# Kernel optimization log

Hardware: AMD Instinct MI355X
Metric: run time of the kernel (lower is better)

## Reference

```python
import jax, jax.numpy as jnp
import numpy as np

B, S, D, H, V, C = 64, 512, 512, 512, 32000, 1000
FF = 1024

def setup_inputs() -> dict:
    key = jax.random.key(0)
    ks = jax.random.split(key, 12)
    s = 0.02
    return {
        "tokens": jax.random.randint(ks[0], (B, S), 0, V),
        "emb": jax.random.normal(ks[1], (V, D), jnp.float32) * s,
        "Wx": jax.random.normal(ks[2], (D, H), jnp.float32) * s,
        "Wh": jax.random.normal(ks[3], (H, H), jnp.float32) * s,
        "b_rnn": jnp.zeros((H,), jnp.float32),
        "W1": jax.random.normal(ks[4], (H, FF), jnp.float32) * s,
        "b1": jnp.zeros((FF,), jnp.float32),
        "W2": jax.random.normal(ks[5], (FF, FF), jnp.float32) * s,
        "b2": jnp.zeros((FF,), jnp.float32),
        "Wo": jax.random.normal(ks[6], (FF, C), jnp.float32) * s,
        "bo": jnp.zeros((C,), jnp.float32),
    }

def reference(tokens, emb, Wx, Wh, b_rnn, W1, b1, W2, b2, Wo, bo):
    # Embedding with mask_zero=True: token 0 is a masked timestep
    x = emb[tokens]                                   # [B,S,D]
    mask = (tokens != 0)                              # [B,S]
    # Precompute input projection for all timesteps (hoisted out of the scan)
    xproj = jnp.einsum('bsd,dh->bsh', x, Wx) + b_rnn  # [B,S,H]

    def step(h, inp):
        xp, m = inp                                   # [B,H], [B]
        h_new = jax.nn.relu(xp + h @ Wh)
        # Keras masking: masked steps carry previous state forward
        h = jnp.where(m[:, None], h_new, h)
        return h, None

    h0 = jnp.zeros((B, H), xproj.dtype)
    h, _ = jax.lax.scan(step, h0, (xproj.transpose(1, 0, 2), mask.T))

    y = jax.nn.relu(h @ W1 + b1)
    y = jax.nn.relu(y @ W2 + b2)
    return jax.nn.softmax(y @ Wo + bo, axis=-1)       # [B,C]
```

## Files before the change

### kernel.cpp

```cpp
#include <hip/hip_runtime.h>
#include <stdint.h>

typedef _Float16 half2_t __attribute__((ext_vector_type(2)));
typedef short bf16x8 __attribute__((ext_vector_type(8)));
typedef float f32x4 __attribute__((ext_vector_type(4)));
typedef int i32x4 __attribute__((ext_vector_type(4)));
typedef int i32x8 __attribute__((ext_vector_type(8)));
typedef unsigned short u16;
typedef unsigned int u32;
typedef unsigned long long u64;

#define B_ 64
#define S_ 512
#define D_ 512
#define H_ 512
#define FF_ 1024
#define C_ 1000
#define V_ 32000

#define SW4 128.0f
#define SH4 256.0f

__device__ __forceinline__ u16 f2bf(float f){
  u32 u = __builtin_bit_cast(u32, f);
  u = (u + 0x7FFFu + ((u >> 16) & 1u)) >> 16;
  return (u16)u;
}
__device__ __forceinline__ u32 pkbf(float a, float b){
  return (u32)f2bf(a) | ((u32)f2bf(b) << 16);
}
__device__ __forceinline__ u32 packh2(float a, float b){
  u16 lo = __builtin_bit_cast(u16, (_Float16)a);
  u16 hi = __builtin_bit_cast(u16, (_Float16)b);
  return (u32)lo | ((u32)hi << 16);
}
__device__ __forceinline__ float fdot2u(u32 a, u32 b, float c){
  return __builtin_amdgcn_fdot2(__builtin_bit_cast(half2_t, a),
                                __builtin_bit_cast(half2_t, b), c, false);
}
__device__ __forceinline__ float h2f(u16 h){
  return (float)__builtin_bit_cast(_Float16, h);
}
__device__ __forceinline__ float fp4val(u32 c){
  int e = (c >> 1) & 3;
  float m = 1.0f + 0.5f * (float)(c & 1);
  return (e == 0) ? 0.5f * (float)(c & 1) : m * (float)(1 << (e - 1));
}

__global__ void k_prep(const float* __restrict__ Wx, u16* __restrict__ WxT,
                       const float* __restrict__ Wh, uint4* __restrict__ Wf4){
  __shared__ u16 t[64][65];
  int bid = blockIdx.x, tid = threadIdx.x;
  if (bid < 64){
    int bx = bid & 7, by = bid >> 3;
    int c = tid & 63, r0 = (tid >> 6) * 16;
    #pragma unroll
    for (int i = 0; i < 16; i++){
      int k = by * 64 + r0 + i, n = bx * 64 + c;
      t[r0 + i][c] = f2bf(Wx[k * 512 + n]);
    }
    __syncthreads();
    #pragma unroll
    for (int i = 0; i < 16; i++){
      int n = bx * 64 + r0 + i, k = by * 64 + c;
      WxT[n * 512 + k] = t[c][r0 + i];
    }
  } else {
    int g = (bid - 64) * 256 + tid;
    int fidx = g >> 6, l = g & 63;
    int wv = fidx >> 4, ct = (fidx >> 2) & 3, kt = fidx & 3;
    int q = l >> 4, n = wv * 64 + ct * 16 + (l & 15);
    int k0 = kt * 128 + q * 32;
    u32 d[4] = {0u, 0u, 0u, 0u};
    #pragma unroll
    for (int j = 0; j < 32; j++){
      float w = Wh[(size_t)(k0 + j) * 512 + n] * SW4;
      float aw = fabsf(w);
      u32 s = (w < 0.f) ? 8u : 0u;
      u32 c;
      if (aw < 2.f) c = (u32)(int)rintf(aw * 2.f);
      else if (aw < 4.f) c = 4u + (u32)(int)rintf(aw - 2.f);
      else { c = 6u + (u32)(int)rintf((aw - 4.f) * 0.5f); if (c > 7u) c = 7u; }
      d[j >> 3] |= (c | s) << (4 * (j & 7));
    }
    uint4 o; o.x = d[0]; o.y = d[1]; o.z = d[2]; o.w = d[3];
    Wf4[(size_t)fidx * 64 + l] = o;
  }
}

__global__ __launch_bounds__(512) void k_gemm(const float* __restrict__ emb,
                                              const u16* __restrict__ WxT,
                                              const float* __restrict__ bias,
                                              u16* __restrict__ xpV,
                                              const float* __restrict__ W1, u32* __restrict__ W1p,
                                              const float* __restrict__ W2, u32* __restrict__ W2p,
                                              const float* __restrict__ Wo, u32* __restrict__ Wop){
  __shared__ __align__(16) u16 As[64 * 40];
  int bid = blockIdx.x, tid = threadIdx.x;
  if (bid >= 500){
    if (bid < 1012){
      int i = (bid - 500) * 512 + tid;
      int p = i >> 10, n = i & 1023;
      W1p[p * FF_ + n] = packh2(W1[(2 * p) * FF_ + n], W1[(2 * p + 1) * FF_ + n]);
    } else if (bid < 2036){
      int i = (bid - 1012) * 512 + tid;
      int p = i >> 10, n = i & 1023;
      W2p[p * FF_ + n] = packh2(W2[(2 * p) * FF_ + n], W2[(2 * p + 1) * FF_ + n]);
    } else {
      int i = (bid - 2036) * 512 + tid;
      int p = i >> 10, n = i & 1023;
      if (n < C_)
        Wop[p * C_ + n] = packh2(Wo[(2 * p) * C_ + n], Wo[(2 * p + 1) * C_ + n]);
    }
    return;
  }
  int m0 = bid * 64;
  int w = tid >> 6, l = tid & 63, kg = l >> 4, r16 = l & 15;
  const u16* bptr[4];
  #pragma unroll
  for (int ni = 0; ni < 4; ni++)
    bptr[ni] = WxT + (size_t)(w * 64 + ni * 16 + r16) * 512 + kg * 8;
  f32x4 acc[4][4];
  #pragma unroll
  for (int mi = 0; mi < 4; mi++)
    #pragma unroll
    for (int ni = 0; ni < 4; ni++) acc[mi][ni] = (f32x4){0.f, 0.f, 0.f, 0.f};
  int srow = tid >> 3, sk = (tid & 7) * 4;
  const float* ebase = emb + (size_t)(m0 + srow) * 512 + sk;
  float4 f = *(const float4*)ebase;
  for (int kt = 0; kt < 16; kt++){
    u32 lo = pkbf(f.x, f.y), hi = pkbf(f.z, f.w);
    float4 fn;
    if (kt < 15) fn = *(const float4*)(ebase + (kt + 1) * 32);
    __syncthreads();
    uint2 st; st.x = lo; st.y = hi;
    *(uint2*)(As + srow * 40 + sk) = st;
    __syncthreads();
    bf16x8 bfr[4], af[4];
    #pragma unroll
    for (int ni = 0; ni < 4; ni++)
      bfr[ni] = *(const bf16x8*)(bptr[ni] + kt * 32);
    #pragma unroll
    for (int mi = 0; mi < 4; mi++)
      af[mi] = *(const bf16x8*)(As + (mi * 16 + r16) * 40 + kg * 8);
    #pragma unroll
    for (int mi = 0; mi < 4; mi++)
      #pragma unroll
      for (int ni = 0; ni < 4; ni++)
        acc[mi][ni] = __builtin_amdgcn_mfma_f32_16x16x32_bf16(af[mi], bfr[ni], acc[mi][ni], 0, 0, 0);
    f = fn;
  }
  #pragma unroll
  for (int ni = 0; ni < 4; ni++){
    int col = w * 64 + ni * 16 + r16;
    float bb = bias[col];
    #pragma unroll
    for (int mi = 0; mi < 4; mi++){
      int mb = m0 + mi * 16 + kg * 4;
      #pragma unroll
      for (int r = 0; r < 4; r++){
        float v = (acc[mi][ni][r] + bb) * SH4;
        xpV[(size_t)(mb + r) * 512 + col] = __builtin_bit_cast(u16, (_Float16)v);
      }
    }
  }
}

__global__ __launch_bounds__(512, 2) void k_rnn(
    const uint4* __restrict__ Wf4, const u16* __restrict__ xpV,
    const int* __restrict__ tokens, u32* __restrict__ hpack){
  __shared__ __align__(16) unsigned char gA[256];
  __shared__ __align__(16) unsigned char gB[256];
  __shared__ int toks[512];
  int b = blockIdx.x, tid = threadIdx.x;
  int wv = tid >> 6, l = tid & 63, q = l >> 4, n16 = l & 15;
  int col = wv * 64 + q * 16 + n16;

  i32x8 wgt[16];
  #pragma unroll
  for (int ct = 0; ct < 4; ct++)
    #pragma unroll
    for (int kt = 0; kt < 4; kt++){
      int fidx = (wv * 4 + ct) * 4 + kt;
      uint4 wl = Wf4[(size_t)fidx * 64 + l];
      i32x8 w8 = {(int)wl.x, (int)wl.y, (int)wl.z, (int)wl.w, 0, 0, 0, 0};
      wgt[ct * 4 + kt] = w8;
    }

  toks[tid] = tokens[b * 512 + tid];
  if (tid < 64) ((u32*)gA)[tid] = 0;
  __syncthreads();

  const u16* xpc = xpV + col;
  u16 xraw = xpc[(size_t)toks[0] * 512];
  u32 greg = 0;

#define RNN_STEP(T, SRC, DST)                                                 \
  {                                                                           \
    int tn = toks[(T + 1) & 511];                                             \
    u16 xnext = xpc[(size_t)tn * 512];                                        \
    bool wr = toks[T] != 0;                                                   \
    i32x4 av0 = *(const i32x4*)(SRC + 0 * 64 + q * 16);                       \
    i32x4 av1 = *(const i32x4*)(SRC + 1 * 64 + q * 16);                       \
    i32x4 av2 = *(const i32x4*)(SRC + 2 * 64 + q * 16);                       \
    i32x4 av3 = *(const i32x4*)(SRC + 3 * 64 + q * 16);                       \
    i32x8 a80 = {av0[0], av0[1], av0[2], av0[3], 0, 0, 0, 0};                 \
    i32x8 a81 = {av1[0], av1[1], av1[2], av1[3], 0, 0, 0, 0};                 \
    i32x8 a82 = {av2[0], av2[1], av2[2], av2[3], 0, 0, 0, 0};                 \
    i32x8 a83 = {av3[0], av3[1], av3[2], av3[3], 0, 0, 0, 0};                 \
    f32x4 acc0 = {0.f,0.f,0.f,0.f}, acc1 = {0.f,0.f,0.f,0.f};                 \
    f32x4 acc2 = {0.f,0.f,0.f,0.f}, acc3 = {0.f,0.f,0.f,0.f};                 \
    __builtin_amdgcn_s_setprio(1);                                            \
    acc0 = __builtin_amdgcn_mfma_scale_f32_16x16x128_f8f6f4(a80, wgt[0],  acc0, 4, 4, 0, 127, 0, 127); \
    acc1 = __builtin_amdgcn_mfma_scale_f32_16x16x128_f8f6f4(a80, wgt[4],  acc1, 4, 4, 0, 127, 0, 127); \
    acc2 = __builtin_amdgcn_mfma_scale_f32_16x16x128_f8f6f4(a80, wgt[8],  acc2, 4, 4, 0, 127, 0, 127); \
    acc3 = __builtin_amdgcn_mfma_scale_f32_16x16x128_f8f6f4(a80, wgt[12], acc3, 4, 4, 0, 127, 0, 127); \
    acc0 = __builtin_amdgcn_mfma_scale_f32_16x16x128_f8f6f4(a81, wgt[1],  acc0, 4, 4, 0, 127, 0, 127); \
    acc1 = __builtin_amdgcn_mfma_scale_f32_16x16x128_f8f6f4(a81, wgt[5],  acc1, 4, 4, 0, 127, 0, 127); \
    acc2 = __builtin_amdgcn_mfma_scale_f32_16x16x128_f8f6f4(a81, wgt[9],  acc2, 4, 4, 0, 127, 0, 127); \
    acc3 = __builtin_amdgcn_mfma_scale_f32_16x16x128_f8f6f4(a81, wgt[13], acc3, 4, 4, 0, 127, 0, 127); \
    acc0 = __builtin_amdgcn_mfma_scale_f32_16x16x128_f8f6f4(a82, wgt[2],  acc0, 4, 4, 0, 127, 0, 127); \
    acc1 = __builtin_amdgcn_mfma_scale_f32_16x16x128_f8f6f4(a82, wgt[6],  acc1, 4, 4, 0, 127, 0, 127); \
    acc2 = __builtin_amdgcn_mfma_scale_f32_16x16x128_f8f6f4(a82, wgt[10], acc2, 4, 4, 0, 127, 0, 127); \
    acc3 = __builtin_amdgcn_mfma_scale_f32_16x16x128_f8f6f4(a82, wgt[14], acc3, 4, 4, 0, 127, 0, 127); \
    acc0 = __builtin_amdgcn_mfma_scale_f32_16x16x128_f8f6f4(a83, wgt[3],  acc0, 4, 4, 0, 127, 0, 127); \
    acc1 = __builtin_amdgcn_mfma_scale_f32_16x16x128_f8f6f4(a83, wgt[7],  acc1, 4, 4, 0, 127, 0, 127); \
    acc2 = __builtin_amdgcn_mfma_scale_f32_16x16x128_f8f6f4(a83, wgt[11], acc2, 4, 4, 0, 127, 0, 127); \
    acc3 = __builtin_amdgcn_mfma_scale_f32_16x16x128_f8f6f4(a83, wgt[15], acc3, 4, 4, 0, 127, 0, 127); \
    __builtin_amdgcn_s_setprio(0);                                            \
    float av = (q == 0) ? acc0[0] : (q == 1) ? acc1[0] : (q == 2) ? acc2[0] : acc3[0]; \
    float gn = fmaxf(fmaf(av, 1.0f / SW4, h2f(xraw)), 0.f);                   \
    u32 code;                                                                 \
    if (gn < 2.f) code = (u32)(int)rintf(gn * 2.f);                           \
    else if (gn < 4.f) code = 4u + (u32)(int)rintf(gn - 2.f);                 \
    else { u32 c = 6u + (u32)(int)rintf((gn - 4.f) * 0.5f); code = c > 7u ? 7u : c; } \
    u32 pc = (u32)__shfl_xor((int)code, 1);                                   \
    u32 byte = (n16 & 1) ? (pc | (code << 4)) : (code | (pc << 4));           \
    if (wr) greg = byte;                                                      \
    if ((l & 1) == 0) DST[col >> 1] = (unsigned char)greg;                    \
    xraw = xnext;                                                             \
  }

  #pragma unroll 1
  for (int t = 0; t < 512; t += 2){
    RNN_STEP(t, gA, gB);
    __syncthreads();
    RNN_STEP(t + 1, gB, gA);
    __syncthreads();
  }
#undef RNN_STEP

  if (tid < 256){
    u32 byte = gA[tid];
    float f0 = fp4val(byte & 15u) * (1.0f / SH4);
    float f1 = fp4val(byte >> 4) * (1.0f / SH4);
    hpack[b * 256 + tid] = packh2(f0, f1);
  }
}

__global__ __launch_bounds__(256) void k_fc1(const u32* __restrict__ hpack,
    const u32* __restrict__ W1p, const float* __restrict__ b1, u32* __restrict__ y1p){
  __shared__ u32 h0[256], h1[256];
  int nx = blockIdx.x, bp = blockIdx.y, tid = threadIdx.x;
  int ba = bp * 2, bb = ba + 1;
  int n = nx * 256 + tid;
  h0[tid] = hpack[ba * 256 + tid];
  h1[tid] = hpack[bb * 256 + tid];
  __syncthreads();
  float a0 = 0.f, a1 = 0.f;
  #pragma unroll 8
  for (int p = 0; p < 256; p++){
    u32 w = W1p[p * FF_ + n];
    a0 = fdot2u(w, h0[p], a0);
    a1 = fdot2u(w, h1[p], a1);
  }
  float bbv = b1[n];
  float y0 = fmaxf(a0 + bbv, 0.f), y1 = fmaxf(a1 + bbv, 0.f);
  float o0 = __shfl_xor(y0, 1), o1 = __shfl_xor(y1, 1);
  if (!(tid & 1)){
    y1p[ba * 512 + (n >> 1)] = packh2(y0, o0);
    y1p[bb * 512 + (n >> 1)] = packh2(y1, o1);
  }
}

__global__ __launch_bounds__(256) void k_fc2(const u32* __restrict__ y1p,
    const u32* __restrict__ W2p, const float* __restrict__ b2, u32* __restrict__ y2p){
  __shared__ u32 h0[512], h1[512];
  int nx = blockIdx.x, bp = blockIdx.y, tid = threadIdx.x;
  int ba = bp * 2, bb = ba + 1;
  int n = nx * 256 + tid;
  h0[tid] = y1p[ba * 512 + tid];       h1[tid] = y1p[bb * 512 + tid];
  h0[tid + 256] = y1p[ba * 512 + 256 + tid];
  h1[tid + 256] = y1p[bb * 512 + 256 + tid];
  __syncthreads();
  float a0 = 0.f, a1 = 0.f;
  #pragma unroll 8
  for (int p = 0; p < 512; p++){
    u32 w = W2p[p * FF_ + n];
    a0 = fdot2u(w, h0[p], a0);
    a1 = fdot2u(w, h1[p], a1);
  }
  float bbv = b2[n];
  float y0 = fmaxf(a0 + bbv, 0.f), y1 = fmaxf(a1 + bbv, 0.f);
  float o0 = __shfl_xor(y0, 1), o1 = __shfl_xor(y1, 1);
  if (!(tid & 1)){
    y2p[ba * 512 + (n >> 1)] = packh2(y0, o0);
    y2p[bb * 512 + (n >> 1)] = packh2(y1, o1);
  }
}

__global__ __launch_bounds__(256) void k_outz(const u32* __restrict__ y2p,
    const u32* __restrict__ Wop, const float* __restrict__ bo, float* __restrict__ z){
  __shared__ u32 h0[512], h1[512];
  int nx = blockIdx.x, bp = blockIdx.y, tid = threadIdx.x;
  int ba = bp * 2, bb = ba + 1;
  h0[tid] = y2p[ba * 512 + tid];       h1[tid] = y2p[bb * 512 + tid];
  h0[tid + 256] = y2p[ba * 512 + 256 + tid];
  h1[tid + 256] = y2p[bb * 512 + 256 + tid];
  __syncthreads();
  int n = nx * 250 + tid;
  if (tid >= 250) return;
  float a0 = 0.f, a1 = 0.f;
  #pragma unroll 8
  for (int p = 0; p < 512; p++){
    u32 w = Wop[p * C_ + n];
    a0 = fdot2u(w, h0[p], a0);
    a1 = fdot2u(w, h1[p], a1);
  }
  float bbv = bo[n];
  z[ba * C_ + n] = a0 + bbv;
  z[bb * C_ + n] = a1 + bbv;
}

__global__ __launch_bounds__(256) void k_norm(const float* __restrict__ z,
                                              float* __restrict__ out){
  __shared__ float redm[4], reds[4];
  int b = blockIdx.x, tid = threadIdx.x;
  float z0 = z[b * C_ + tid];
  float z1 = z[b * C_ + 256 + tid];
  float z2 = z[b * C_ + 512 + tid];
  bool v3 = (768 + tid) < C_;
  float z3 = v3 ? z[b * C_ + 768 + tid] : -1e30f;
  float mx = fmaxf(fmaxf(z0, z1), fmaxf(z2, z3));
  #pragma unroll
  for (int o = 1; o < 64; o <<= 1) mx = fmaxf(mx, __shfl_xor(mx, o));
  if ((tid & 63) == 0) redm[tid >> 6] = mx;
  __syncthreads();
  mx = fmaxf(fmaxf(redm[0], redm[1]), fmaxf(redm[2], redm[3]));
  float e0 = __expf(z0 - mx), e1 = __expf(z1 - mx), e2 = __expf(z2 - mx);
  float e3 = v3 ? __expf(z3 - mx) : 0.f;
  float s = e0 + e1 + e2 + e3;
  #pragma unroll
  for (int o = 1; o < 64; o <<= 1) s += __shfl_xor(s, o);
  if ((tid & 63) == 0) reds[tid >> 6] = s;
  __syncthreads();
  s = reds[0] + reds[1] + reds[2] + reds[3];
  float inv = 1.0f / s;
  out[b * C_ + tid] = e0 * inv;
  out[b * C_ + 256 + tid] = e1 * inv;
  out[b * C_ + 512 + tid] = e2 * inv;
  if (v3) out[b * C_ + 768 + tid] = e3 * inv;
}

extern "C" void kernel_launch(void* const* d_in, const int* in_sizes, int n_in,
                              void* d_out, int out_size, void* d_ws, size_t ws_size,
                              hipStream_t stream) {
  const int*   tokens = (const int*)d_in[0];
  const float* emb    = (const float*)d_in[1];
  const float* Wx     = (const float*)d_in[2];
  const float* Wh     = (const float*)d_in[3];
  const float* brnn   = (const float*)d_in[4];
  const float* W1     = (const float*)d_in[5];
  const float* b1     = (const float*)d_in[6];
  const float* W2     = (const float*)d_in[7];
  const float* b2     = (const float*)d_in[8];
  const float* Wo     = (const float*)d_in[9];
  const float* bo     = (const float*)d_in[10];
  float* out = (float*)d_out;

  char* ws = (char*)d_ws;
  size_t off = 0;
  auto alloc = [&](size_t bytes) -> void* {
    void* p = ws + off;
    off += (bytes + 255) & ~(size_t)255;
    return p;
  };
  u16* WxT    = (u16*)alloc((size_t)512 * 512 * 2);
  u16* xpV    = (u16*)alloc((size_t)V_ * 512 * 2);
  uint4* Wf4  = (uint4*)alloc((size_t)128 * 64 * 16);
  u32* W1p    = (u32*)alloc((size_t)256 * 1024 * 4);
  u32* W2p    = (u32*)alloc((size_t)512 * 1024 * 4);
  u32* Wop    = (u32*)alloc((size_t)512 * 1000 * 4);
  u32* hpack  = (u32*)alloc((size_t)64 * 256 * 4);
  u32* y1p    = (u32*)alloc((size_t)64 * 512 * 4);
  u32* y2p    = (u32*)alloc((size_t)64 * 512 * 4);
  float* zbuf = (float*)alloc((size_t)64 * 1000 * 4);

  k_prep<<<dim3(96), dim3(256), 0, stream>>>(Wx, WxT, Wh, Wf4);
  k_gemm<<<dim3(3060), dim3(512), 0, stream>>>(emb, WxT, brnn, xpV,
                                               W1, W1p, W2, W2p, Wo, Wop);
  k_rnn<<<dim3(64), dim3(512), 0, stream>>>(Wf4, xpV, tokens, hpack);
  k_fc1<<<dim3(4, 32), dim3(256), 0, stream>>>(hpack, W1p, b1, y1p);
  k_fc2<<<dim3(4, 32), dim3(256), 0, stream>>>(y1p, W2p, b2, y2p);
  k_outz<<<dim3(4, 32), dim3(256), 0, stream>>>(y2p, Wop, bo, zbuf);
  k_norm<<<dim3(64), dim3(256), 0, stream>>>(zbuf, out);
}
```

Before: 377.3 us.

## Switch RNN hidden state to FP8 and fuse MLP tail into one grid-barrier kernel

```diff
diff --git a/kernel.cpp b/kernel.cpp
--- a/kernel.cpp
+++ b/kernel.cpp
@@ -40,11 +40,6 @@
 }
 __device__ __forceinline__ float h2f(u16 h){
   return (float)__builtin_bit_cast(_Float16, h);
-}
-__device__ __forceinline__ float fp4val(u32 c){
-  int e = (c >> 1) & 3;
-  float m = 1.0f + 0.5f * (float)(c & 1);
-  return (e == 0) ? 0.5f * (float)(c & 1) : m * (float)(1 << (e - 1));
 }
 
 __global__ void k_prep(const float* __restrict__ Wx, u16* __restrict__ WxT,
@@ -94,10 +89,12 @@
                                               u16* __restrict__ xpV,
                                               const float* __restrict__ W1, u32* __restrict__ W1p,
                                               const float* __restrict__ W2, u32* __restrict__ W2p,
-                                              const float* __restrict__ Wo, u32* __restrict__ Wop){
+                                              const float* __restrict__ Wo, u32* __restrict__ Wop,
+                                              u32* __restrict__ sync){
   __shared__ __align__(16) u16 As[64 * 40];
   int bid = blockIdx.x, tid = threadIdx.x;
   if (bid >= 500){
+    if (bid == 500 && tid < 8) sync[tid] = 0;
     if (bid < 1012){
       int i = (bid - 500) * 512 + tid;
       int p = i >> 10, n = i & 1023;
@@ -169,8 +166,8 @@
 __global__ __launch_bounds__(512, 2) void k_rnn(
     const uint4* __restrict__ Wf4, const u16* __restrict__ xpV,
     const int* __restrict__ tokens, u32* __restrict__ hpack){
-  __shared__ __align__(16) unsigned char gA[256];
-  __shared__ __align__(16) unsigned char gB[256];
+  __shared__ __align__(32) unsigned char gA[512];
+  __shared__ __align__(32) unsigned char gB[512];
   __shared__ int toks[512];
   int b = blockIdx.x, tid = threadIdx.x;
   int wv = tid >> 6, l = tid & 63, q = l >> 4, n16 = l & 15;
@@ -188,7 +185,7 @@
     }
 
   toks[tid] = tokens[b * 512 + tid];
-  if (tid < 64) ((u32*)gA)[tid] = 0;
+  if (tid < 128) ((u32*)gA)[tid] = 0;
   __syncthreads();
 
   const u16* xpc = xpV + col;
@@ -200,44 +197,35 @@
     int tn = toks[(T + 1) & 511];                                             \
     u16 xnext = xpc[(size_t)tn * 512];                                        \
     bool wr = toks[T] != 0;                                                   \
-    i32x4 av0 = *(const i32x4*)(SRC + 0 * 64 + q * 16);                       \
-    i32x4 av1 = *(const i32x4*)(SRC + 1 * 64 + q * 16);                       \
-    i32x4 av2 = *(const i32x4*)(SRC + 2 * 64 + q * 16);                       \
-    i32x4 av3 = *(const i32x4*)(SRC + 3 * 64 + q * 16);                       \
-    i32x8 a80 = {av0[0], av0[1], av0[2], av0[3], 0, 0, 0, 0};                 \
-    i32x8 a81 = {av1[0], av1[1], av1[2], av1[3], 0, 0, 0, 0};                 \
-    i32x8 a82 = {av2[0], av2[1], av2[2], av2[3], 0, 0, 0, 0};                 \
-    i32x8 a83 = {av3[0], av3[1], av3[2], av3[3], 0, 0, 0, 0};                 \
+    i32x8 a80 = *(const i32x8*)(SRC + 0 * 128 + q * 32);                      \
+    i32x8 a81 = *(const i32x8*)(SRC + 1 * 128 + q * 32);                      \
+    i32x8 a82 = *(const i32x8*)(SRC + 2 * 128 + q * 32);                      \
+    i32x8 a83 = *(const i32x8*)(SRC + 3 * 128 + q * 32);                      \
     f32x4 acc0 = {0.f,0.f,0.f,0.f}, acc1 = {0.f,0.f,0.f,0.f};                 \
     f32x4 acc2 = {0.f,0.f,0.f,0.f}, acc3 = {0.f,0.f,0.f,0.f};                 \
     __builtin_amdgcn_s_setprio(1);                                            \
-    acc0 = __builtin_amdgcn_mfma_scale_f32_16x16x128_f8f6f4(a80, wgt[0],  acc0, 4, 4, 0, 127, 0, 127); \
-    acc1 = __builtin_amdgcn_mfma_scale_f32_16x16x128_f8f6f4(a80, wgt[4],  acc1, 4, 4, 0, 127, 0, 127); \
-    acc2 = __builtin_amdgcn_mfma_scale_f32_16x16x128_f8f6f4(a80, wgt[8],  acc2, 4, 4, 0, 127, 0, 127); \
-    acc3 = __builtin_amdgcn_mfma_scale_f32_16x16x128_f8f6f4(a80, wgt[12], acc3, 4, 4, 0, 127, 0, 127); \
-    acc0 = __builtin_amdgcn_mfma_scale_f32_16x16x128_f8f6f4(a81, wgt[1],  acc0, 4, 4, 0, 127, 0, 127); \
-    acc1 = __builtin_amdgcn_mfma_scale_f32_16x16x128_f8f6f4(a81, wgt[5],  acc1, 4, 4, 0, 127, 0, 127); \
-    acc2 = __builtin_amdgcn_mfma_scale_f32_16x16x128_f8f6f4(a81, wgt[9],  acc2, 4, 4, 0, 127, 0, 127); \
-    acc3 = __builtin_amdgcn_mfma_scale_f32_16x16x128_f8f6f4(a81, wgt[13], acc3, 4, 4, 0, 127, 0, 127); \
-    acc0 = __builtin_amdgcn_mfma_scale_f32_16x16x128_f8f6f4(a82, wgt[2],  acc0, 4, 4, 0, 127, 0, 127); \
-    acc1 = __builtin_amdgcn_mfma_scale_f32_16x16x128_f8f6f4(a82, wgt[6],  acc1, 4, 4, 0, 127, 0, 127); \
-    acc2 = __builtin_amdgcn_mfma_scale_f32_16x16x128_f8f6f4(a82, wgt[10], acc2, 4, 4, 0, 127, 0, 127); \
-    acc3 = __builtin_amdgcn_mfma_scale_f32_16x16x128_f8f6f4(a82, wgt[14], acc3, 4, 4, 0, 127, 0, 127); \
-    acc0 = __builtin_amdgcn_mfma_scale_f32_16x16x128_f8f6f4(a83, wgt[3],  acc0, 4, 4, 0, 127, 0, 127); \
-    acc1 = __builtin_amdgcn_mfma_scale_f32_16x16x128_f8f6f4(a83, wgt[7],  acc1, 4, 4, 0, 127, 0, 127); \
-    acc2 = __builtin_amdgcn_mfma_scale_f32_16x16x128_f8f6f4(a83, wgt[11], acc2, 4, 4, 0, 127, 0, 127); \
-    acc3 = __builtin_amdgcn_mfma_scale_f32_16x16x128_f8f6f4(a83, wgt[15], acc3, 4, 4, 0, 127, 0, 127); \
+    acc0 = __builtin_amdgcn_mfma_scale_f32_16x16x128_f8f6f4(a80, wgt[0],  acc0, 0, 4, 0, 127, 0, 127); \
+    acc1 = __builtin_amdgcn_mfma_scale_f32_16x16x128_f8f6f4(a80, wgt[4],  acc1, 0, 4, 0, 127, 0, 127); \
+    acc2 = __builtin_amdgcn_mfma_scale_f32_16x16x128_f8f6f4(a80, wgt[8],  acc2, 0, 4, 0, 127, 0, 127); \
+    acc3 = __builtin_amdgcn_mfma_scale_f32_16x16x128_f8f6f4(a80, wgt[12], acc3, 0, 4, 0, 127, 0, 127); \
+    acc0 = __builtin_amdgcn_mfma_scale_f32_16x16x128_f8f6f4(a81, wgt[1],  acc0, 0, 4, 0, 127, 0, 127); \
+    acc1 = __builtin_amdgcn_mfma_scale_f32_16x16x128_f8f6f4(a81, wgt[5],  acc1, 0, 4, 0, 127, 0, 127); \
+    acc2 = __builtin_amdgcn_mfma_scale_f32_16x16x128_f8f6f4(a81, wgt[9],  acc2, 0, 4, 0, 127, 0, 127); \
+    acc3 = __builtin_amdgcn_mfma_scale_f32_16x16x128_f8f6f4(a81, wgt[13], acc3, 0, 4, 0, 127, 0, 127); \
+    acc0 = __builtin_amdgcn_mfma_scale_f32_16x16x128_f8f6f4(a82, wgt[2],  acc0, 0, 4, 0, 127, 0, 127); \
+    acc1 = __builtin_amdgcn_mfma_scale_f32_16x16x128_f8f6f4(a82, wgt[6],  acc1, 0, 4, 0, 127, 0, 127); \
+    acc2 = __builtin_amdgcn_mfma_scale_f32_16x16x128_f8f6f4(a82, wgt[10], acc2, 0, 4, 0, 127, 0, 127); \
+    acc3 = __builtin_amdgcn_mfma_scale_f32_16x16x128_f8f6f4(a82, wgt[14], acc3, 0, 4, 0, 127, 0, 127); \
+    acc0 = __builtin_amdgcn_mfma_scale_f32_16x16x128_f8f6f4(a83, wgt[3],  acc0, 0, 4, 0, 127, 0, 127); \
+    acc1 = __builtin_amdgcn_mfma_scale_f32_16x16x128_f8f6f4(a83, wgt[7],  acc1, 0, 4, 0, 127, 0, 127); \
+    acc2 = __builtin_amdgcn_mfma_scale_f32_16x16x128_f8f6f4(a83, wgt[11], acc2, 0, 4, 0, 127, 0, 127); \
+    acc3 = __builtin_amdgcn_mfma_scale_f32_16x16x128_f8f6f4(a83, wgt[15], acc3, 0, 4, 0, 127, 0, 127); \
     __builtin_amdgcn_s_setprio(0);                                            \
     float av = (q == 0) ? acc0[0] : (q == 1) ? acc1[0] : (q == 2) ? acc2[0] : acc3[0]; \
     float gn = fmaxf(fmaf(av, 1.0f / SW4, h2f(xraw)), 0.f);                   \
-    u32 code;                                                                 \
-    if (gn < 2.f) code = (u32)(int)rintf(gn * 2.f);                           \
-    else if (gn < 4.f) code = 4u + (u32)(int)rintf(gn - 2.f);                 \
-    else { u32 c = 6u + (u32)(int)rintf((gn - 4.f) * 0.5f); code = c > 7u ? 7u : c; } \
-    u32 pc = (u32)__shfl_xor((int)code, 1);                                   \
-    u32 byte = (n16 & 1) ? (pc | (code << 4)) : (code | (pc << 4));           \
-    if (wr) greg = byte;                                                      \
-    if ((l & 1) == 0) DST[col >> 1] = (unsigned char)greg;                    \
+    u32 pk = __builtin_amdgcn_cvt_pk_fp8_f32(gn, gn, 0, false) & 0xFFu;       \
+    if (wr) greg = pk;                                                        \
+    DST[col] = (unsigned char)greg;                                           \
     xraw = xnext;                                                             \
   }
 
@@ -251,115 +239,129 @@
 #undef RNN_STEP
 
   if (tid < 256){
-    u32 byte = gA[tid];
-    float f0 = fp4val(byte & 15u) * (1.0f / SH4);
-    float f1 = fp4val(byte >> 4) * (1.0f / SH4);
+    u32 two = *(const u16*)(gA + 2 * tid);
+    float f0 = __builtin_amdgcn_cvt_f32_fp8(two, 0) * (1.0f / SH4);
+    float f1 = __builtin_amdgcn_cvt_f32_fp8(two, 1) * (1.0f / SH4);
     hpack[b * 256 + tid] = packh2(f0, f1);
   }
 }
 
-__global__ __launch_bounds__(256) void k_fc1(const u32* __restrict__ hpack,
-    const u32* __restrict__ W1p, const float* __restrict__ b1, u32* __restrict__ y1p){
-  __shared__ u32 h0[256], h1[256];
-  int nx = blockIdx.x, bp = blockIdx.y, tid = threadIdx.x;
+__device__ __forceinline__ void gridbar(u32* cnt, u32 target){
+  __threadfence();
+  __syncthreads();
+  if (threadIdx.x == 0){
+    atomicAdd(cnt, 1u);
+    while (atomicAdd(cnt, 0u) < target) __builtin_amdgcn_s_sleep(2);
+  }
+  __syncthreads();
+  __threadfence();
+}
+
+__global__ __launch_bounds__(256, 1) void k_tailm(const u32* __restrict__ hpack,
+    const u32* __restrict__ W1p, const float* __restrict__ b1,
+    const u32* __restrict__ W2p, const float* __restrict__ b2,
+    const u32* __restrict__ Wop, const float* __restrict__ bo,
+    u32* __restrict__ y1p, u32* __restrict__ y2p,
+    float* __restrict__ zbuf, float* __restrict__ out, u32* __restrict__ sync){
+  __shared__ u32 h0[512], h1[512];
+  __shared__ float redm[4], reds[4];
+  int bid = blockIdx.x, tid = threadIdx.x;
+  int nx = bid & 3, bp = bid >> 2;
   int ba = bp * 2, bb = ba + 1;
-  int n = nx * 256 + tid;
-  h0[tid] = hpack[ba * 256 + tid];
-  h1[tid] = hpack[bb * 256 + tid];
-  __syncthreads();
-  float a0 = 0.f, a1 = 0.f;
-  #pragma unroll 8
-  for (int p = 0; p < 256; p++){
-    u32 w = W1p[p * FF_ + n];
-    a0 = fdot2u(w, h0[p], a0);
-    a1 = fdot2u(w, h1[p], a1);
-  }
-  float bbv = b1[n];
-  float y0 = fmaxf(a0 + bbv, 0.f), y1 = fmaxf(a1 + bbv, 0.f);
-  float o0 = __shfl_xor(y0, 1), o1 = __shfl_xor(y1, 1);
-  if (!(tid & 1)){
-    y1p[ba * 512 + (n >> 1)] = packh2(y0, o0);
-    y1p[bb * 512 + (n >> 1)] = packh2(y1, o1);
-  }
-}
-
-__global__ __launch_bounds__(256) void k_fc2(const u32* __restrict__ y1p,
-    const u32* __restrict__ W2p, const float* __restrict__ b2, u32* __restrict__ y2p){
-  __shared__ u32 h0[512], h1[512];
-  int nx = blockIdx.x, bp = blockIdx.y, tid = threadIdx.x;
-  int ba = bp * 2, bb = ba + 1;
-  int n = nx * 256 + tid;
-  h0[tid] = y1p[ba * 512 + tid];       h1[tid] = y1p[bb * 512 + tid];
-  h0[tid + 256] = y1p[ba * 512 + 256 + tid];
-  h1[tid + 256] = y1p[bb * 512 + 256 + tid];
-  __syncthreads();
-  float a0 = 0.f, a1 = 0.f;
-  #pragma unroll 8
-  for (int p = 0; p < 512; p++){
-    u32 w = W2p[p * FF_ + n];
-    a0 = fdot2u(w, h0[p], a0);
-    a1 = fdot2u(w, h1[p], a1);
-  }
-  float bbv = b2[n];
-  float y0 = fmaxf(a0 + bbv, 0.f), y1 = fmaxf(a1 + bbv, 0.f);
-  float o0 = __shfl_xor(y0, 1), o1 = __shfl_xor(y1, 1);
-  if (!(tid & 1)){
-    y2p[ba * 512 + (n >> 1)] = packh2(y0, o0);
-    y2p[bb * 512 + (n >> 1)] = packh2(y1, o1);
-  }
-}
-
-__global__ __launch_bounds__(256) void k_outz(const u32* __restrict__ y2p,
-    const u32* __restrict__ Wop, const float* __restrict__ bo, float* __restrict__ z){
-  __shared__ u32 h0[512], h1[512];
-  int nx = blockIdx.x, bp = blockIdx.y, tid = threadIdx.x;
-  int ba = bp * 2, bb = ba + 1;
-  h0[tid] = y2p[ba * 512 + tid];       h1[tid] = y2p[bb * 512 + tid];
-  h0[tid + 256] = y2p[ba * 512 + 256 + tid];
-  h1[tid + 256] = y2p[bb * 512 + 256 + tid];
-  __syncthreads();
-  int n = nx * 250 + tid;
-  if (tid >= 250) return;
-  float a0 = 0.f, a1 = 0.f;
-  #pragma unroll 8
-  for (int p = 0; p < 512; p++){
-    u32 w = Wop[p * C_ + n];
-    a0 = fdot2u(w, h0[p], a0);
-    a1 = fdot2u(w, h1[p], a1);
-  }
-  float bbv = bo[n];
-  z[ba * C_ + n] = a0 + bbv;
-  z[bb * C_ + n] = a1 + bbv;
-}
-
-__global__ __launch_bounds__(256) void k_norm(const float* __restrict__ z,
-                                              float* __restrict__ out){
-  __shared__ float redm[4], reds[4];
-  int b = blockIdx.x, tid = threadIdx.x;
-  float z0 = z[b * C_ + tid];
-  float z1 = z[b * C_ + 256 + tid];
-  float z2 = z[b * C_ + 512 + tid];
-  bool v3 = (768 + tid) < C_;
-  float z3 = v3 ? z[b * C_ + 768 + tid] : -1e30f;
-  float mx = fmaxf(fmaxf(z0, z1), fmaxf(z2, z3));
-  #pragma unroll
-  for (int o = 1; o < 64; o <<= 1) mx = fmaxf(mx, __shfl_xor(mx, o));
-  if ((tid & 63) == 0) redm[tid >> 6] = mx;
-  __syncthreads();
-  mx = fmaxf(fmaxf(redm[0], redm[1]), fmaxf(redm[2], redm[3]));
-  float e0 = __expf(z0 - mx), e1 = __expf(z1 - mx), e2 = __expf(z2 - mx);
-  float e3 = v3 ? __expf(z3 - mx) : 0.f;
-  float s = e0 + e1 + e2 + e3;
-  #pragma unroll
-  for (int o = 1; o < 64; o <<= 1) s += __shfl_xor(s, o);
-  if ((tid & 63) == 0) reds[tid >> 6] = s;
-  __syncthreads();
-  s = reds[0] + reds[1] + reds[2] + reds[3];
-  float inv = 1.0f / s;
-  out[b * C_ + tid] = e0 * inv;
-  out[b * C_ + 256 + tid] = e1 * inv;
-  out[b * C_ + 512 + tid] = e2 * inv;
-  if (v3) out[b * C_ + 768 + tid] = e3 * inv;
+
+  {
+    h0[tid] = hpack[ba * 256 + tid];
+    h1[tid] = hpack[bb * 256 + tid];
+    __syncthreads();
+    int n = nx * 256 + tid;
+    float a0 = 0.f, a1 = 0.f;
+    #pragma unroll 8
+    for (int p = 0; p < 256; p++){
+      u32 w = W1p[p * FF_ + n];
+      a0 = fdot2u(w, h0[p], a0);
+      a1 = fdot2u(w, h1[p], a1);
+    }
+    float bbv = b1[n];
+    float y0 = fmaxf(a0 + bbv, 0.f), y1 = fmaxf(a1 + bbv, 0.f);
+    float o0 = __shfl_xor(y0, 1), o1 = __shfl_xor(y1, 1);
+    if (!(tid & 1)){
+      y1p[ba * 512 + (n >> 1)] = packh2(y0, o0);
+      y1p[bb * 512 + (n >> 1)] = packh2(y1, o1);
+    }
+  }
+  gridbar(sync + 0, 128);
+
+  {
+    h0[tid] = y1p[ba * 512 + tid];       h1[tid] = y1p[bb * 512 + tid];
+    h0[tid + 256] = y1p[ba * 512 + 256 + tid];
+    h1[tid + 256] = y1p[bb * 512 + 256 + tid];
+    __syncthreads();
+    int n = nx * 256 + tid;
+    float a0 = 0.f, a1 = 0.f;
+    #pragma unroll 8
+    for (int p = 0; p < 512; p++){
+      u32 w = W2p[p * FF_ + n];
+      a0 = fdot2u(w, h0[p], a0);
+      a1 = fdot2u(w, h1[p], a1);
+    }
+    float bbv = b2[n];
+    float y0 = fmaxf(a0 + bbv, 0.f), y1 = fmaxf(a1 + bbv, 0.f);
+    float o0 = __shfl_xor(y0, 1), o1 = __shfl_xor(y1, 1);
+    if (!(tid & 1)){
+      y2p[ba * 512 + (n >> 1)] = packh2(y0, o0);
+      y2p[bb * 512 + (n >> 1)] = packh2(y1, o1);
+    }
+  }
+  gridbar(sync + 1, 128);
+
+  {
+    h0[tid] = y2p[ba * 512 + tid];       h1[tid] = y2p[bb * 512 + tid];
+    h0[tid + 256] = y2p[ba * 512 + 256 + tid];
+    h1[tid + 256] = y2p[bb * 512 + 256 + tid];
+    __syncthreads();
+    if (tid < 250){
+      int n = nx * 250 + tid;
+      float a0 = 0.f, a1 = 0.f;
+      #pragma unroll 8
+      for (int p = 0; p < 512; p++){
+        u32 w = Wop[p * C_ + n];
+        a0 = fdot2u(w, h0[p], a0);
+        a1 = fdot2u(w, h1[p], a1);
+      }
+      float bbv = bo[n];
+      zbuf[ba * C_ + n] = a0 + bbv;
+      zbuf[bb * C_ + n] = a1 + bbv;
+    }
+  }
+  gridbar(sync + 2, 128);
+
+  if (bid < 64){
+    int b = bid;
+    float z0 = zbuf[b * C_ + tid];
+    float z1 = zbuf[b * C_ + 256 + tid];
+    float z2 = zbuf[b * C_ + 512 + tid];
+    bool v3 = (768 + tid) < C_;
+    float z3 = v3 ? zbuf[b * C_ + 768 + tid] : -1e30f;
+    float mx = fmaxf(fmaxf(z0, z1), fmaxf(z2, z3));
+    #pragma unroll
+    for (int o = 1; o < 64; o <<= 1) mx = fmaxf(mx, __shfl_xor(mx, o));
+    if ((tid & 63) == 0) redm[tid >> 6] = mx;
+    __syncthreads();
+    mx = fmaxf(fmaxf(redm[0], redm[1]), fmaxf(redm[2], redm[3]));
+    float e0 = __expf(z0 - mx), e1 = __expf(z1 - mx), e2 = __expf(z2 - mx);
+    float e3 = v3 ? __expf(z3 - mx) : 0.f;
+    float s = e0 + e1 + e2 + e3;
+    #pragma unroll
+    for (int o = 1; o < 64; o <<= 1) s += __shfl_xor(s, o);
+    if ((tid & 63) == 0) reds[tid >> 6] = s;
+    __syncthreads();
+    s = reds[0] + reds[1] + reds[2] + reds[3];
+    float inv = 1.0f / s;
+    out[b * C_ + tid] = e0 * inv;
+    out[b * C_ + 256 + tid] = e1 * inv;
+    out[b * C_ + 512 + tid] = e2 * inv;
+    if (v3) out[b * C_ + 768 + tid] = e3 * inv;
+  }
 }
 
 extern "C" void kernel_launch(void* const* d_in, const int* in_sizes, int n_in,
@@ -395,13 +397,12 @@
   u32* y1p    = (u32*)alloc((size_t)64 * 512 * 4);
   u32* y2p    = (u32*)alloc((size_t)64 * 512 * 4);
   float* zbuf = (float*)alloc((size_t)64 * 1000 * 4);
+  u32* sync   = (u32*)alloc(256);
 
   k_prep<<<dim3(96), dim3(256), 0, stream>>>(Wx, WxT, Wh, Wf4);
   k_gemm<<<dim3(3060), dim3(512), 0, stream>>>(emb, WxT, brnn, xpV,
-                                               W1, W1p, W2, W2p, Wo, Wop);
+                                               W1, W1p, W2, W2p, Wo, Wop, sync);
   k_rnn<<<dim3(64), dim3(512), 0, stream>>>(Wf4, xpV, tokens, hpack);
-  k_fc1<<<dim3(4, 32), dim3(256), 0, stream>>>(hpack, W1p, b1, y1p);
-  k_fc2<<<dim3(4, 32), dim3(256), 0, stream>>>(y1p, W2p, b2, y2p);
-  k_outz<<<dim3(4, 32), dim3(256), 0, stream>>>(y2p, Wop, bo, zbuf);
-  k_norm<<<dim3(64), dim3(256), 0, stream>>>(zbuf, out);
-}
+  k_tailm<<<dim3(128), dim3(256), 0, stream>>>(hpack, W1p, b1, W2p, b2, Wop, bo,
+                                               y1p, y2p, zbuf, out, sync);
+}
```

Result: slower. 504.1 us (+33.6%).
